# Performance work log

Hardware: AMD Instinct MI355X
Metric: run time of the kernel (lower is better)

The kernel has to match this reference:

```python
import jax, jax.numpy as jnp
import numpy as np

N, E = 40000, 640000
IN, HID, OUT = 128, 128, 128


def _lin(key, fan_in, fan_out):
    bound = 1.0 / np.sqrt(fan_in)
    kw, kb = jax.random.split(key)
    W = jax.random.uniform(kw, (fan_in, fan_out), jnp.float32, -bound, bound)
    b = jax.random.uniform(kb, (fan_out,), jnp.float32, -bound, bound)
    return W, b


def setup_inputs() -> dict:
    key = jax.random.key(0)
    ks = jax.random.split(key, 10)
    node_feat = jax.random.normal(ks[0], (N, IN), jnp.float32)
    coord_feat = jax.random.normal(ks[1], (N, 3), jnp.float32)
    src = jax.random.randint(ks[2], (E,), 0, N, jnp.int32)
    dst = jax.random.randint(ks[3], (E,), 0, N, jnp.int32)
    # edge_mlp: Linear(2*IN+1 -> HID), SiLU, Linear(HID -> HID), SiLU
    We1, be1 = _lin(ks[4], 2 * IN + 1, HID)
    We2, be2 = _lin(ks[5], HID, HID)
    # node_mlp: Linear(IN+HID -> HID), SiLU, Linear(HID -> OUT)
    Wn1, bn1 = _lin(ks[6], IN + HID, HID)
    Wn2, bn2 = _lin(ks[7], HID, OUT)
    # coord_mlp: Linear(HID -> HID), SiLU, Linear(HID -> 1, bias=False)
    Wc1, bc1 = _lin(ks[8], HID, HID)
    Wc2, _ = _lin(ks[9], HID, 1)
    return {"node_feat": node_feat, "coord_feat": coord_feat, "src": src, "dst": dst,
            "We1": We1, "be1": be1, "We2": We2, "be2": be2,
            "Wn1": Wn1, "bn1": bn1, "Wn2": Wn2, "bn2": bn2,
            "Wc1": Wc1, "bc1": bc1, "Wc2": Wc2}


def reference(node_feat, coord_feat, src, dst,
              We1, be1, We2, be2, Wn1, bn1, Wn2, bn2, Wc1, bc1, Wc2):
    n = node_feat.shape[0]
    # edge gather: u_sub_v gives x_src - x_dst
    x_diff = coord_feat[src] - coord_feat[dst]                       # (E, 3)
    dist = jnp.sqrt(jnp.sum(x_diff * x_diff, axis=-1, keepdims=True))  # (E, 1)
    x_dir = x_diff / (dist + 1e-7)
    f = jnp.concatenate([node_feat[src], node_feat[dst], dist], axis=-1)  # (E, 2*IN+1)
    msg_h = jax.nn.silu(jax.nn.silu(f @ We1 + be1) @ We2 + be2)      # (E, HID)
    coef = jax.nn.silu(msg_h @ Wc1 + bc1) @ Wc2                      # (E, 1)
    msg_x = coef * x_dir                                             # (E, 3)
    # scatter-reduce to destination nodes: sum for h, mean for x
    h_neigh = jax.ops.segment_sum(msg_h, dst, num_segments=n)        # (N, HID)
    cnt = jax.ops.segment_sum(jnp.ones((dst.shape[0], 1), msg_x.dtype), dst, num_segments=n)
    x_neigh = jax.ops.segment_sum(msg_x, dst, num_segments=n) / jnp.maximum(cnt, 1.0)
    h = jax.nn.silu(jnp.concatenate([node_feat, h_neigh], axis=-1) @ Wn1 + bn1) @ Wn2 + bn2
    return h, coord_feat + x_neigh
```

## Files before the change

### kernel.cpp

```cpp
#include <hip/hip_runtime.h>
#include <hip/hip_bf16.h>
#include <math.h>
#include <stdint.h>

#define N_NODES 40000
#define N_EDGES 640000

typedef short short8 __attribute__((ext_vector_type(8)));
typedef float f32x4 __attribute__((ext_vector_type(4)));

__device__ __forceinline__ float silu(float x) {
    return __fdividef(x, 1.0f + __expf(-x));
}

__device__ __forceinline__ unsigned short f2bf(float f) {
    unsigned u = __float_as_uint(f);
    u += 0x7FFF + ((u >> 16) & 1);
    return (unsigned short)(u >> 16);
}
__device__ __forceinline__ float bf2f(unsigned short h) {
    return __uint_as_float(((unsigned)h) << 16);
}
__device__ __forceinline__ unsigned pk2bf(float a, float b) {
    __hip_bfloat162 h = __float22bfloat162_rn(make_float2(a, b));
    unsigned u;
    __builtin_memcpy(&u, &h, 4);
    return u;
}

__global__ __launch_bounds__(1024) void k_scanA(const int* __restrict__ deg,
                                                int* __restrict__ rsl,
                                                int* __restrict__ btot) {
    __shared__ int wsum[16];
    const int t = threadIdx.x;
    const int lane = t & 63, wid = t >> 6;
    const int base = blockIdx.x * 1000;
    const int x0 = (t < 1000) ? deg[base + t] : 0;
    int x = x0;
#pragma unroll
    for (int s = 1; s < 64; s <<= 1) {
        const int u = __shfl_up(x, s, 64);
        if (lane >= s) x += u;
    }
    if (lane == 63) wsum[wid] = x;
    __syncthreads();
    if (wid == 0) {
        int ws = (lane < 16) ? wsum[lane] : 0;
#pragma unroll
        for (int s = 1; s < 16; s <<= 1) {
            const int u = __shfl_up(ws, s, 64);
            if (lane >= s) ws += u;
        }
        if (lane < 16) wsum[lane] = ws;
    }
    __syncthreads();
    const int wbase = (wid > 0) ? wsum[wid - 1] : 0;
    if (t < 1000) rsl[base + t] = wbase + x - x0;
    if (t == 0) btot[blockIdx.x] = wsum[15];
}

__global__ __launch_bounds__(256) void k_fill(const int* __restrict__ dst,
                                              const int* __restrict__ rsl,
                                              const int* __restrict__ btot,
                                              int* __restrict__ cursor,
                                              int* __restrict__ elist) {
    __shared__ int sbo[40];
    const int t = threadIdx.x;
    if (t < 64) {
        const int x0 = (t < 40) ? btot[t] : 0;
        int x = x0;
#pragma unroll
        for (int s = 1; s < 64; s <<= 1) {
            const int u = __shfl_up(x, s, 64);
            if (t >= s) x += u;
        }
        if (t < 40) sbo[t] = x - x0;
    }
    __syncthreads();
    const int e = blockIdx.x * 256 + t;
    if (e < N_EDGES) {
        const int d = dst[e];
        const int p = atomicAdd(&cursor[d], 1);
        elist[sbo[d / 1000] + rsl[d] + p] = e;
    }
}

__global__ __launch_bounds__(128) void k_pack2(
    const float* __restrict__ We1, const float* __restrict__ We2,
    const float* __restrict__ Wc1, const float* __restrict__ Wn1,
    const float* __restrict__ Wn2,
    unsigned short* __restrict__ Wt_e1, unsigned short* __restrict__ Wt_e2,
    unsigned short* __restrict__ Wt_c1, unsigned short* __restrict__ Wt_n1,
    unsigned short* __restrict__ Wt_n2,
    int* __restrict__ deg, int* __restrict__ cursor, float* __restrict__ xs,
    float* __restrict__ hn) {
    const int b = blockIdx.x;
    const int t = threadIdx.x;
    Wt_e1[b * 128 + t] = f2bf(We1[(size_t)((b >> 7) * 128 + t) * 128 + (b & 127)]);
    if (b < 128) {
        Wt_e2[b * 128 + t] = f2bf(We2[(size_t)t * 128 + b]);
        Wt_c1[b * 128 + t] = f2bf(Wc1[(size_t)t * 128 + b]);
        Wt_n2[b * 128 + t] = f2bf(Wn2[(size_t)t * 128 + b]);
        Wt_n1[b * 256 + t] = f2bf(Wn1[(size_t)t * 128 + b]);
        Wt_n1[b * 256 + 128 + t] = f2bf(Wn1[(size_t)(128 + t) * 128 + b]);
    }
    const int gid = b * 128 + t;
    for (int i = gid; i < N_NODES; i += 32768) { deg[i] = 0; cursor[i] = 0; }
    for (int i = gid; i < N_NODES * 4; i += 32768) xs[i] = 0.0f;
    float4* hz = (float4*)hn;
    const float4 z4 = {0.f, 0.f, 0.f, 0.f};
    for (int i = gid; i < N_NODES * 32; i += 32768) hz[i] = z4;
}

__global__ __launch_bounds__(256) void k_cntpre(
    const float* __restrict__ nf, const unsigned short* __restrict__ Wt_e1,
    const float* __restrict__ be1,
    unsigned short* __restrict__ Pc,
    const int* __restrict__ dst, int* __restrict__ deg) {
    __shared__ __align__(16) unsigned short sNF[32][136];
    const int t = threadIdx.x;
    const int node0 = blockIdx.x * 32;
    {
        const int e0 = (blockIdx.x * 256 + t) * 2;
        const int d0 = dst[e0], d1 = dst[e0 + 1];
        atomicAdd(&deg[d0], 1);
        atomicAdd(&deg[d1], 1);
    }
    {
        const int m = t >> 3, kc = (t & 7) * 16;
        const float* sp = &nf[(size_t)(node0 + m) * 128 + kc];
        const float4 v0 = *(const float4*)(sp + 0);
        const float4 v1 = *(const float4*)(sp + 4);
        const float4 v2 = *(const float4*)(sp + 8);
        const float4 v3 = *(const float4*)(sp + 12);
        int4 o0, o1;
        o0.x = pk2bf(v0.x, v0.y); o0.y = pk2bf(v0.z, v0.w);
        o0.z = pk2bf(v1.x, v1.y); o0.w = pk2bf(v1.z, v1.w);
        o1.x = pk2bf(v2.x, v2.y); o1.y = pk2bf(v2.z, v2.w);
        o1.z = pk2bf(v3.x, v3.y); o1.w = pk2bf(v3.z, v3.w);
        *(int4*)&sNF[m][kc] = o0;
        *(int4*)&sNF[m][kc + 8] = o1;
    }
    __syncthreads();

    const int w = t >> 6, l = t & 63, c = l & 15, quad = l >> 4;
    const int n0 = w * 64;

    f32x4 acc[2][4];
#pragma unroll
    for (int mt = 0; mt < 2; mt++)
#pragma unroll
        for (int tl = 0; tl < 4; tl++) acc[mt][tl] = (f32x4){0.f, 0.f, 0.f, 0.f};

#pragma unroll
    for (int k0 = 0; k0 < 128; k0 += 32) {
        const short8 a0 = *(const short8*)&sNF[c][k0 + quad * 8];
        const short8 a1 = *(const short8*)&sNF[16 + c][k0 + quad * 8];
#pragma unroll
        for (int tl = 0; tl < 4; tl++) {
            const short8 b = *(const short8*)(Wt_e1 +
                ((size_t)(n0 + tl * 16 + c) << 7) + k0 + quad * 8);
            acc[0][tl] = __builtin_amdgcn_mfma_f32_16x16x32_bf16(a0, b, acc[0][tl], 0, 0, 0);
            acc[1][tl] = __builtin_amdgcn_mfma_f32_16x16x32_bf16(a1, b, acc[1][tl], 0, 0, 0);
        }
    }
#pragma unroll
    for (int mt = 0; mt < 2; mt++)
#pragma unroll
        for (int tl = 0; tl < 4; tl++) {
            const int col = n0 + tl * 16 + c;
            const float bias = (col >= 128) ? be1[col - 128] : 0.0f;
            const unsigned p01 = pk2bf(acc[mt][tl][0] + bias, acc[mt][tl][1] + bias);
            const unsigned p23 = pk2bf(acc[mt][tl][2] + bias, acc[mt][tl][3] + bias);
            const int row = node0 + mt * 16 + quad * 4;
            Pc[(size_t)(row + 0) * 256 + col] = (unsigned short)p01;
            Pc[(size_t)(row + 1) * 256 + col] = (unsigned short)(p01 >> 16);
            Pc[(size_t)(row + 2) * 256 + col] = (unsigned short)p23;
            Pc[(size_t)(row + 3) * 256 + col] = (unsigned short)(p23 >> 16);
        }
}

__global__ __launch_bounds__(256) void k_edge9(
    const unsigned short* __restrict__ Pc, const float* __restrict__ coord,
    const int* __restrict__ src, const int* __restrict__ dst,
    const int* __restrict__ elist,
    const float* __restrict__ We1,
    const unsigned short* __restrict__ Wt_e2, const float* __restrict__ be2,
    const unsigned short* __restrict__ Wt_c1, const float* __restrict__ bc1,
    const float* __restrict__ Wc2,
    float* __restrict__ h_neigh, float* __restrict__ xs) {
    __shared__ __align__(16) unsigned short sT[64][136];
    __shared__ float scoefp[4][32];
    __shared__ float sw[128];
    __shared__ float sdist[64];
    __shared__ float sxd[64][3];
    __shared__ int ssrc[64];
    __shared__ int sdst[64];

    const int t = threadIdx.x;
    const int bid = (int)blockIdx.x;
    const int swz = (bid & 7) * 1250 + (bid >> 3);
    const int e0 = swz * 64;

    if (t < 64) {
        const int eid = elist[e0 + t];
        const int s = src[eid], d = dst[eid];
        ssrc[t] = s; sdst[t] = d;
        const float dx = coord[3 * s + 0] - coord[3 * d + 0];
        const float dy = coord[3 * s + 1] - coord[3 * d + 1];
        const float dz = coord[3 * s + 2] - coord[3 * d + 2];
        const float dist = sqrtf(dx * dx + dy * dy + dz * dz);
        sdist[t] = dist;
        const float inv = __fdividef(1.0f, dist + 1e-7f);
        sxd[t][0] = dx * inv; sxd[t][1] = dy * inv; sxd[t][2] = dz * inv;
    } else if (t < 96) {
        ((float4*)sw)[t - 64] = ((const float4*)(We1 + 256 * 128))[t - 64];
    }
    __syncthreads();

    {
        const int e = t >> 2;
        const int kc = (t & 3) * 32;
        const int s = ssrc[e], d = sdst[e];
        const float dist = sdist[e];
        const unsigned short* p1 = Pc + (size_t)s * 256 + kc;
        const unsigned short* p2 = Pc + (size_t)d * 256 + 128 + kc;
        short8 a[4], b[4];
#pragma unroll
        for (int i = 0; i < 4; i++) {
            a[i] = *(const short8*)(p1 + i * 8);
            b[i] = *(const short8*)(p2 + i * 8);
        }
#pragma unroll
        for (int i = 0; i < 4; i++) {
            float v[8];
#pragma unroll
            for (int kk = 0; kk < 8; kk++) {
                const int k = kc + i * 8 + kk;
                v[kk] = silu(bf2f((unsigned short)a[i][kk]) + bf2f((unsigned short)b[i][kk])
                             + dist * sw[k]);
            }
            int4 o;
            o.x = pk2bf(v[0], v[1]); o.y = pk2bf(v[2], v[3]);
            o.z = pk2bf(v[4], v[5]); o.w = pk2bf(v[6], v[7]);
            *(int4*)&sT[e][kc + i * 8] = o;
        }
    }
    __syncthreads();

    const int w = t >> 6;
    const int l = t & 63;
    const int h = w & 1;
    const int H = w >> 1;
    const int m0 = h * 32;
    const int n0 = H * 64;
    const int c = l & 15;
    const int quad = l >> 4;

    f32x4 acc1[2][4];
#pragma unroll
    for (int mt = 0; mt < 2; mt++)
#pragma unroll
        for (int tile = 0; tile < 4; tile++) acc1[mt][tile] = (f32x4){0.f, 0.f, 0.f, 0.f};
#pragma unroll
    for (int k0 = 0; k0 < 128; k0 += 32) {
        const short8 a0 = *(const short8*)&sT[m0 + c][k0 + quad * 8];
        const short8 a1 = *(const short8*)&sT[m0 + 16 + c][k0 + quad * 8];
#pragma unroll
        for (int tile = 0; tile < 4; tile++) {
            const short8 b = *(const short8*)(Wt_e2 +
                ((size_t)(n0 + tile * 16 + c) << 7) + k0 + quad * 8);
            acc1[0][tile] = __builtin_amdgcn_mfma_f32_16x16x32_bf16(a0, b, acc1[0][tile], 0, 0, 0);
            acc1[1][tile] = __builtin_amdgcn_mfma_f32_16x16x32_bf16(a1, b, acc1[1][tile], 0, 0, 0);
        }
    }
    __syncthreads();

#pragma unroll
    for (int mt = 0; mt < 2; mt++)
#pragma unroll
        for (int tile = 0; tile < 4; tile++) {
            const int col = n0 + tile * 16 + c;
            const float bb = be2[col];
            const unsigned p01 = pk2bf(silu(acc1[mt][tile][0] + bb), silu(acc1[mt][tile][1] + bb));
            const unsigned p23 = pk2bf(silu(acc1[mt][tile][2] + bb), silu(acc1[mt][tile][3] + bb));
            const int row = m0 + mt * 16 + quad * 4;
            sT[row + 0][col] = (unsigned short)p01;
            sT[row + 1][col] = (unsigned short)(p01 >> 16);
            sT[row + 2][col] = (unsigned short)p23;
            sT[row + 3][col] = (unsigned short)(p23 >> 16);
        }
    __syncthreads();

    {
        const int j = t & 127;
        const int q = t >> 7;
        const int eb = q * 32;
        float aA = bf2f(sT[eb][j]);      int pA = sdst[eb];
        float aB = bf2f(sT[eb + 16][j]); int pB = sdst[eb + 16];
#pragma unroll
        for (int i = 1; i < 16; i++) {
            const int dA = sdst[eb + i];
            const int dB = sdst[eb + 16 + i];
            const float vA = bf2f(sT[eb + i][j]);
            const float vB = bf2f(sT[eb + 16 + i][j]);
            if (dA != pA) { atomicAdd(&h_neigh[(size_t)pA * 128 + j], aA); aA = 0.f; pA = dA; }
            aA += vA;
            if (dB != pB) { atomicAdd(&h_neigh[(size_t)pB * 128 + j], aB); aB = 0.f; pB = dB; }
            aB += vB;
        }
        atomicAdd(&h_neigh[(size_t)pA * 128 + j], aA);
        atomicAdd(&h_neigh[(size_t)pB * 128 + j], aB);
    }

    {
        f32x4 acc[2][4];
#pragma unroll
        for (int mt = 0; mt < 2; mt++)
#pragma unroll
            for (int tile = 0; tile < 4; tile++) acc[mt][tile] = (f32x4){0.f, 0.f, 0.f, 0.f};
#pragma unroll
        for (int k0 = 0; k0 < 128; k0 += 32) {
            const short8 a0 = *(const short8*)&sT[m0 + c][k0 + quad * 8];
            const short8 a1 = *(const short8*)&sT[m0 + 16 + c][k0 + quad * 8];
#pragma unroll
            for (int tile = 0; tile < 4; tile++) {
                const short8 b = *(const short8*)(Wt_c1 +
                    ((size_t)(n0 + tile * 16 + c) << 7) + k0 + quad * 8);
                acc[0][tile] = __builtin_amdgcn_mfma_f32_16x16x32_bf16(a0, b, acc[0][tile], 0, 0, 0);
                acc[1][tile] = __builtin_amdgcn_mfma_f32_16x16x32_bf16(a1, b, acc[1][tile], 0, 0, 0);
            }
        }
        float part[2][4] = {{0.f, 0.f, 0.f, 0.f}, {0.f, 0.f, 0.f, 0.f}};
#pragma unroll
        for (int tile = 0; tile < 4; tile++) {
            const int col = n0 + tile * 16 + c;
            const float bc = bc1[col];
            const float wc = Wc2[col];
#pragma unroll
            for (int mt = 0; mt < 2; mt++)
#pragma unroll
                for (int r = 0; r < 4; r++)
                    part[mt][r] += silu(acc[mt][tile][r] + bc) * wc;
        }
#pragma unroll
        for (int off = 1; off < 16; off <<= 1) {
#pragma unroll
            for (int mt = 0; mt < 2; mt++)
#pragma unroll
                for (int r = 0; r < 4; r++)
                    part[mt][r] += __shfl_xor(part[mt][r], off, 64);
        }
        if (c == 0) {
#pragma unroll
            for (int mt = 0; mt < 2; mt++)
#pragma unroll
                for (int r = 0; r < 4; r++)
                    scoefp[w][mt * 16 + quad * 4 + r] = part[mt][r];
        }
    }

    if (l < 32) {
        const int e = h * 32 + l;
        const int d = sdst[e];
        const float cf = scoefp[w][l];
        float v0 = cf * sxd[e][0];
        float v1 = cf * sxd[e][1];
        float v2 = cf * sxd[e][2];
#pragma unroll
        for (int s = 1; s < 32; s <<= 1) {
            const float u0 = __shfl_down(v0, s, 64);
            const float u1 = __shfl_down(v1, s, 64);
            const float u2 = __shfl_down(v2, s, 64);
            const int ud = __shfl_down(d, s, 64);
            if (l + s < 32 && ud == d) { v0 += u0; v1 += u1; v2 += u2; }
        }
        if (l == 0 || sdst[e - 1] != d) {
            atomicAdd(&xs[(size_t)d * 4 + 0], v0);
            atomicAdd(&xs[(size_t)d * 4 + 1], v1);
            atomicAdd(&xs[(size_t)d * 4 + 2], v2);
        }
    }
}

__global__ __launch_bounds__(256) void k_node(
    const float* __restrict__ nf, const float* __restrict__ coord,
    const float* __restrict__ hn, const float* __restrict__ xs,
    const int* __restrict__ deg,
    const unsigned short* __restrict__ Wt_n1, const float* __restrict__ bn1,
    const unsigned short* __restrict__ Wt_n2, const float* __restrict__ bn2,
    float* __restrict__ out_h, float* __restrict__ out_x) {
    __shared__ __align__(16) unsigned short sAB[32][264];
    __shared__ __align__(16) unsigned short sH[32][136];
    const int t = threadIdx.x;
    const int node0 = blockIdx.x * 32;
    {
        const int m = t >> 3, kc = (t & 7) * 32;
        const float* base = (kc < 128) ? &nf[(size_t)(node0 + m) * 128 + kc]
                                       : &hn[(size_t)(node0 + m) * 128 + (kc - 128)];
#pragma unroll
        for (int kk = 0; kk < 32; kk += 8) {
            const float4 v0 = *(const float4*)(base + kk);
            const float4 v1 = *(const float4*)(base + kk + 4);
            int4 o;
            o.x = pk2bf(v0.x, v0.y); o.y = pk2bf(v0.z, v0.w);
            o.z = pk2bf(v1.x, v1.y); o.w = pk2bf(v1.z, v1.w);
            *(int4*)&sAB[m][kc + kk] = o;
        }
    }
    if (t < 96) {
        const int m = t / 3, cc = t - m * 3;
        const int i = node0 + m;
        const float cnt = (float)deg[i];
        out_x[(size_t)i * 3 + cc] =
            coord[(size_t)i * 3 + cc] + __fdividef(xs[(size_t)i * 4 + cc], fmaxf(cnt, 1.0f));
    }
    __syncthreads();

    const int w = t >> 6, l = t & 63, c = l & 15, quad = l >> 4;
    const int n0 = w * 32;

    {
        f32x4 acc[2][2];
#pragma unroll
        for (int mt = 0; mt < 2; mt++)
#pragma unroll
            for (int tl = 0; tl < 2; tl++) acc[mt][tl] = (f32x4){0.f, 0.f, 0.f, 0.f};
#pragma unroll
        for (int k0 = 0; k0 < 256; k0 += 32) {
            const short8 a0 = *(const short8*)&sAB[c][k0 + quad * 8];
            const short8 a1 = *(const short8*)&sAB[16 + c][k0 + quad * 8];
#pragma unroll
            for (int tl = 0; tl < 2; tl++) {
                const short8 b = *(const short8*)(Wt_n1 +
                    ((size_t)(n0 + tl * 16 + c) << 8) + k0 + quad * 8);
                acc[0][tl] = __builtin_amdgcn_mfma_f32_16x16x32_bf16(a0, b, acc[0][tl], 0, 0, 0);
                acc[1][tl] = __builtin_amdgcn_mfma_f32_16x16x32_bf16(a1, b, acc[1][tl], 0, 0, 0);
            }
        }
#pragma unroll
        for (int mt = 0; mt < 2; mt++)
#pragma unroll
            for (int tl = 0; tl < 2; tl++) {
                const int col = n0 + tl * 16 + c;
                const float bb = bn1[col];
                const unsigned p01 = pk2bf(silu(acc[mt][tl][0] + bb), silu(acc[mt][tl][1] + bb));
                const unsigned p23 = pk2bf(silu(acc[mt][tl][2] + bb), silu(acc[mt][tl][3] + bb));
                const int row = mt * 16 + quad * 4;
                sH[row + 0][col] = (unsigned short)p01;
                sH[row + 1][col] = (unsigned short)(p01 >> 16);
                sH[row + 2][col] = (unsigned short)p23;
                sH[row + 3][col] = (unsigned short)(p23 >> 16);
            }
    }
    __syncthreads();

    {
        f32x4 acc[2][2];
#pragma unroll
        for (int mt = 0; mt < 2; mt++)
#pragma unroll
            for (int tl = 0; tl < 2; tl++) acc[mt][tl] = (f32x4){0.f, 0.f, 0.f, 0.f};
#pragma unroll
        for (int k0 = 0; k0 < 128; k0 += 32) {
            const short8 a0 = *(const short8*)&sH[c][k0 + quad * 8];
            const short8 a1 = *(const short8*)&sH[16 + c][k0 + quad * 8];
#pragma unroll
            for (int tl = 0; tl < 2; tl++) {
                const short8 b = *(const short8*)(Wt_n2 +
                    ((size_t)(n0 + tl * 16 + c) << 7) + k0 + quad * 8);
                acc[0][tl] = __builtin_amdgcn_mfma_f32_16x16x32_bf16(a0, b, acc[0][tl], 0, 0, 0);
                acc[1][tl] = __builtin_amdgcn_mfma_f32_16x16x32_bf16(a1, b, acc[1][tl], 0, 0, 0);
            }
        }
#pragma unroll
        for (int mt = 0; mt < 2; mt++)
#pragma unroll
            for (int tl = 0; tl < 2; tl++) {
                const int col = n0 + tl * 16 + c;
                const float bb = bn2[col];
#pragma unroll
                for (int r = 0; r < 4; r++) {
                    const int row = mt * 16 + quad * 4 + r;
                    out_h[(size_t)(node0 + row) * 128 + col] = acc[mt][tl][r] + bb;
                }
            }
    }
}

extern "C" void kernel_launch(void* const* d_in, const int* in_sizes, int n_in,
                              void* d_out, int out_size, void* d_ws, size_t ws_size,
                              hipStream_t stream) {
    const float* nf    = (const float*)d_in[0];
    const float* coord = (const float*)d_in[1];
    const int*   src   = (const int*)d_in[2];
    const int*   dst   = (const int*)d_in[3];
    const float* We1   = (const float*)d_in[4];
    const float* be1   = (const float*)d_in[5];
    const float* We2   = (const float*)d_in[6];
    const float* be2   = (const float*)d_in[7];
    const float* Wn1   = (const float*)d_in[8];
    const float* bn1   = (const float*)d_in[9];
    const float* Wn2   = (const float*)d_in[10];
    const float* bn2   = (const float*)d_in[11];
    const float* Wc1   = (const float*)d_in[12];
    const float* bc1   = (const float*)d_in[13];
    const float* Wc2   = (const float*)d_in[14];

    unsigned short* Pc = (unsigned short*)d_ws;
    float* hn = (float*)(Pc + (size_t)N_NODES * 256);
    float* xs = hn + (size_t)N_NODES * 128;
    int* deg       = (int*)(xs + (size_t)N_NODES * 4);
    int* rsl       = deg + N_NODES;
    int* cursor    = rsl + N_NODES;
    int* btot      = cursor + N_NODES;
    int* elist     = btot + 64;
    unsigned short* Wt_e1 = (unsigned short*)
        (((uintptr_t)(elist + N_EDGES) + 255) & ~(uintptr_t)255);
    unsigned short* Wt_e2 = Wt_e1 + 256 * 128;
    unsigned short* Wt_c1 = Wt_e2 + 128 * 128;
    unsigned short* Wt_n1 = Wt_c1 + 128 * 128;
    unsigned short* Wt_n2 = Wt_n1 + 128 * 256;

    float* out_h = (float*)d_out;
    float* out_x = out_h + (size_t)N_NODES * 128;

    k_pack2<<<256, 128, 0, stream>>>(We1, We2, Wc1, Wn1, Wn2,
                                     Wt_e1, Wt_e2, Wt_c1, Wt_n1, Wt_n2,
                                     deg, cursor, xs, hn);
    k_cntpre<<<N_NODES / 32, 256, 0, stream>>>(nf, Wt_e1, be1, Pc, dst, deg);
    k_scanA<<<40, 1024, 0, stream>>>(deg, rsl, btot);
    k_fill<<<(N_EDGES + 255) / 256, 256, 0, stream>>>(dst, rsl, btot, cursor, elist);
    k_edge9<<<N_EDGES / 64, 256, 0, stream>>>(Pc, coord, src, dst, elist,
                                              We1, Wt_e2, be2, Wt_c1, bc1,
                                              Wc2, hn, xs);
    k_node<<<N_NODES / 32, 256, 0, stream>>>(nf, coord, hn, xs, deg,
                                             Wt_n1, bn1, Wt_n2, bn2, out_h, out_x);
}
```

Baseline: 413.4 us.

## Make each wavefront own 16 edges and keep first MLP activations in registers

The edge kernel is reorganized so each of the four wavefronts handles its own 16 edges across all 128 output columns, instead of splitting a 64-edge tile in 2x2 across waves. The first-layer SiLU activations are built straight into MFMA A-operand registers rather than staged through shared memory, and the distance weight row is read from global memory. This removes several block-wide barriers and shared-memory round trips, relying on wave-local lgkmcnt waits. In exchange each wave loads the full Wt_e2 and Wt_c1 B operands (twice the weight traffic per edge), and the correctness of the wave-local waits depends on each wave only touching its own shared rows.

```diff
diff --git a/kernel.cpp b/kernel.cpp
--- a/kernel.cpp
+++ b/kernel.cpp
@@ -180,7 +180,7 @@
         }
 }
 
-__global__ __launch_bounds__(256) void k_edge9(
+__global__ __launch_bounds__(256) void k_edge10(
     const unsigned short* __restrict__ Pc, const float* __restrict__ coord,
     const int* __restrict__ src, const int* __restrict__ dst,
     const int* __restrict__ elist,
@@ -190,120 +190,103 @@
     const float* __restrict__ Wc2,
     float* __restrict__ h_neigh, float* __restrict__ xs) {
     __shared__ __align__(16) unsigned short sT[64][136];
-    __shared__ float scoefp[4][32];
-    __shared__ float sw[128];
+    __shared__ float scoef[4][16];
     __shared__ float sdist[64];
     __shared__ float sxd[64][3];
     __shared__ int ssrc[64];
     __shared__ int sdst[64];
 
     const int t = threadIdx.x;
+    const int w = t >> 6, l = t & 63;
+    const int c = l & 15, quad = l >> 4;
     const int bid = (int)blockIdx.x;
     const int swz = (bid & 7) * 1250 + (bid >> 3);
     const int e0 = swz * 64;
-
-    if (t < 64) {
-        const int eid = elist[e0 + t];
+    const int eb = w * 16;
+
+    if (l < 16) {
+        const int eid = elist[e0 + eb + l];
         const int s = src[eid], d = dst[eid];
-        ssrc[t] = s; sdst[t] = d;
+        ssrc[eb + l] = s; sdst[eb + l] = d;
         const float dx = coord[3 * s + 0] - coord[3 * d + 0];
         const float dy = coord[3 * s + 1] - coord[3 * d + 1];
         const float dz = coord[3 * s + 2] - coord[3 * d + 2];
         const float dist = sqrtf(dx * dx + dy * dy + dz * dz);
-        sdist[t] = dist;
+        sdist[eb + l] = dist;
         const float inv = __fdividef(1.0f, dist + 1e-7f);
-        sxd[t][0] = dx * inv; sxd[t][1] = dy * inv; sxd[t][2] = dz * inv;
-    } else if (t < 96) {
-        ((float4*)sw)[t - 64] = ((const float4*)(We1 + 256 * 128))[t - 64];
-    }
-    __syncthreads();
-
-    {
-        const int e = t >> 2;
-        const int kc = (t & 3) * 32;
-        const int s = ssrc[e], d = sdst[e];
-        const float dist = sdist[e];
-        const unsigned short* p1 = Pc + (size_t)s * 256 + kc;
-        const unsigned short* p2 = Pc + (size_t)d * 256 + 128 + kc;
-        short8 a[4], b[4];
-#pragma unroll
-        for (int i = 0; i < 4; i++) {
-            a[i] = *(const short8*)(p1 + i * 8);
-            b[i] = *(const short8*)(p2 + i * 8);
-        }
-#pragma unroll
-        for (int i = 0; i < 4; i++) {
+        sxd[eb + l][0] = dx * inv; sxd[eb + l][1] = dy * inv; sxd[eb + l][2] = dz * inv;
+    }
+    asm volatile("s_waitcnt lgkmcnt(0)" ::: "memory");
+
+    short8 aQ[4];
+    {
+        const int er = eb + c;
+        const int s = ssrc[er], d = sdst[er];
+        const float dist = sdist[er];
+        const unsigned short* p1 = Pc + (size_t)s * 256 + quad * 8;
+        const unsigned short* p2 = Pc + (size_t)d * 256 + 128 + quad * 8;
+        const float* wd = We1 + 256 * 128 + quad * 8;
+#pragma unroll
+        for (int k0 = 0; k0 < 4; k0++) {
+            const short8 a = *(const short8*)(p1 + k0 * 32);
+            const short8 b = *(const short8*)(p2 + k0 * 32);
+            const float4 w0 = *(const float4*)(wd + k0 * 32);
+            const float4 w1 = *(const float4*)(wd + k0 * 32 + 4);
             float v[8];
-#pragma unroll
-            for (int kk = 0; kk < 8; kk++) {
-                const int k = kc + i * 8 + kk;
-                v[kk] = silu(bf2f((unsigned short)a[i][kk]) + bf2f((unsigned short)b[i][kk])
-                             + dist * sw[k]);
-            }
+            v[0] = silu(bf2f((unsigned short)a[0]) + bf2f((unsigned short)b[0]) + dist * w0.x);
+            v[1] = silu(bf2f((unsigned short)a[1]) + bf2f((unsigned short)b[1]) + dist * w0.y);
+            v[2] = silu(bf2f((unsigned short)a[2]) + bf2f((unsigned short)b[2]) + dist * w0.z);
+            v[3] = silu(bf2f((unsigned short)a[3]) + bf2f((unsigned short)b[3]) + dist * w0.w);
+            v[4] = silu(bf2f((unsigned short)a[4]) + bf2f((unsigned short)b[4]) + dist * w1.x);
+            v[5] = silu(bf2f((unsigned short)a[5]) + bf2f((unsigned short)b[5]) + dist * w1.y);
+            v[6] = silu(bf2f((unsigned short)a[6]) + bf2f((unsigned short)b[6]) + dist * w1.z);
+            v[7] = silu(bf2f((unsigned short)a[7]) + bf2f((unsigned short)b[7]) + dist * w1.w);
             int4 o;
             o.x = pk2bf(v[0], v[1]); o.y = pk2bf(v[2], v[3]);
             o.z = pk2bf(v[4], v[5]); o.w = pk2bf(v[6], v[7]);
-            *(int4*)&sT[e][kc + i * 8] = o;
-        }
-    }
-    __syncthreads();
-
-    const int w = t >> 6;
-    const int l = t & 63;
-    const int h = w & 1;
-    const int H = w >> 1;
-    const int m0 = h * 32;
-    const int n0 = H * 64;
-    const int c = l & 15;
-    const int quad = l >> 4;
-
-    f32x4 acc1[2][4];
-#pragma unroll
-    for (int mt = 0; mt < 2; mt++)
-#pragma unroll
-        for (int tile = 0; tile < 4; tile++) acc1[mt][tile] = (f32x4){0.f, 0.f, 0.f, 0.f};
-#pragma unroll
-    for (int k0 = 0; k0 < 128; k0 += 32) {
-        const short8 a0 = *(const short8*)&sT[m0 + c][k0 + quad * 8];
-        const short8 a1 = *(const short8*)&sT[m0 + 16 + c][k0 + quad * 8];
-#pragma unroll
-        for (int tile = 0; tile < 4; tile++) {
+            __builtin_memcpy(&aQ[k0], &o, 16);
+        }
+    }
+
+    f32x4 acc1[8];
+#pragma unroll
+    for (int tl = 0; tl < 8; tl++) acc1[tl] = (f32x4){0.f, 0.f, 0.f, 0.f};
+#pragma unroll
+    for (int k0 = 0; k0 < 4; k0++) {
+#pragma unroll
+        for (int tl = 0; tl < 8; tl++) {
             const short8 b = *(const short8*)(Wt_e2 +
-                ((size_t)(n0 + tile * 16 + c) << 7) + k0 + quad * 8);
-            acc1[0][tile] = __builtin_amdgcn_mfma_f32_16x16x32_bf16(a0, b, acc1[0][tile], 0, 0, 0);
-            acc1[1][tile] = __builtin_amdgcn_mfma_f32_16x16x32_bf16(a1, b, acc1[1][tile], 0, 0, 0);
-        }
-    }
-    __syncthreads();
-
-#pragma unroll
-    for (int mt = 0; mt < 2; mt++)
-#pragma unroll
-        for (int tile = 0; tile < 4; tile++) {
-            const int col = n0 + tile * 16 + c;
-            const float bb = be2[col];
-            const unsigned p01 = pk2bf(silu(acc1[mt][tile][0] + bb), silu(acc1[mt][tile][1] + bb));
-            const unsigned p23 = pk2bf(silu(acc1[mt][tile][2] + bb), silu(acc1[mt][tile][3] + bb));
-            const int row = m0 + mt * 16 + quad * 4;
-            sT[row + 0][col] = (unsigned short)p01;
-            sT[row + 1][col] = (unsigned short)(p01 >> 16);
-            sT[row + 2][col] = (unsigned short)p23;
-            sT[row + 3][col] = (unsigned short)(p23 >> 16);
-        }
+                ((size_t)(tl * 16 + c) << 7) + k0 * 32 + quad * 8);
+            acc1[tl] = __builtin_amdgcn_mfma_f32_16x16x32_bf16(aQ[k0], b, acc1[tl], 0, 0, 0);
+        }
+    }
+
+#pragma unroll
+    for (int tl = 0; tl < 8; tl++) {
+        const int col = tl * 16 + c;
+        const float bb = be2[col];
+        const unsigned p01 = pk2bf(silu(acc1[tl][0] + bb), silu(acc1[tl][1] + bb));
+        const unsigned p23 = pk2bf(silu(acc1[tl][2] + bb), silu(acc1[tl][3] + bb));
+        const int row = eb + quad * 4;
+        sT[row + 0][col] = (unsigned short)p01;
+        sT[row + 1][col] = (unsigned short)(p01 >> 16);
+        sT[row + 2][col] = (unsigned short)p23;
+        sT[row + 3][col] = (unsigned short)(p23 >> 16);
+    }
     __syncthreads();
 
     {
         const int j = t & 127;
         const int q = t >> 7;
-        const int eb = q * 32;
-        float aA = bf2f(sT[eb][j]);      int pA = sdst[eb];
-        float aB = bf2f(sT[eb + 16][j]); int pB = sdst[eb + 16];
+        const int ebq = q * 32;
+        float aA = bf2f(sT[ebq][j]);      int pA = sdst[ebq];
+        float aB = bf2f(sT[ebq + 16][j]); int pB = sdst[ebq + 16];
 #pragma unroll
         for (int i = 1; i < 16; i++) {
-            const int dA = sdst[eb + i];
-            const int dB = sdst[eb + 16 + i];
-            const float vA = bf2f(sT[eb + i][j]);
-            const float vB = bf2f(sT[eb + 16 + i][j]);
+            const int dA = sdst[ebq + i];
+            const int dB = sdst[ebq + 16 + i];
+            const float vA = bf2f(sT[ebq + i][j]);
+            const float vB = bf2f(sT[ebq + 16 + i][j]);
             if (dA != pA) { atomicAdd(&h_neigh[(size_t)pA * 128 + j], aA); aA = 0.f; pA = dA; }
             aA += vA;
             if (dB != pB) { atomicAdd(&h_neigh[(size_t)pB * 128 + j], aB); aB = 0.f; pB = dB; }
@@ -314,71 +297,66 @@
     }
 
     {
-        f32x4 acc[2][4];
-#pragma unroll
-        for (int mt = 0; mt < 2; mt++)
-#pragma unroll
-            for (int tile = 0; tile < 4; tile++) acc[mt][tile] = (f32x4){0.f, 0.f, 0.f, 0.f};
-#pragma unroll
-        for (int k0 = 0; k0 < 128; k0 += 32) {
-            const short8 a0 = *(const short8*)&sT[m0 + c][k0 + quad * 8];
-            const short8 a1 = *(const short8*)&sT[m0 + 16 + c][k0 + quad * 8];
-#pragma unroll
-            for (int tile = 0; tile < 4; tile++) {
+        short8 a2[4];
+#pragma unroll
+        for (int k0 = 0; k0 < 4; k0++)
+            a2[k0] = *(const short8*)&sT[eb + c][k0 * 32 + quad * 8];
+
+        f32x4 acc2[8];
+#pragma unroll
+        for (int tl = 0; tl < 8; tl++) acc2[tl] = (f32x4){0.f, 0.f, 0.f, 0.f};
+#pragma unroll
+        for (int k0 = 0; k0 < 4; k0++) {
+#pragma unroll
+            for (int tl = 0; tl < 8; tl++) {
                 const short8 b = *(const short8*)(Wt_c1 +
-                    ((size_t)(n0 + tile * 16 + c) << 7) + k0 + quad * 8);
-                acc[0][tile] = __builtin_amdgcn_mfma_f32_16x16x32_bf16(a0, b, acc[0][tile], 0, 0, 0);
-                acc[1][tile] = __builtin_amdgcn_mfma_f32_16x16x32_bf16(a1, b, acc[1][tile], 0, 0, 0);
+                    ((size_t)(tl * 16 + c) << 7) + k0 * 32 + quad * 8);
+                acc2[tl] = __builtin_amdgcn_mfma_f32_16x16x32_bf16(a2[k0], b, acc2[tl], 0, 0, 0);
             }
         }
-        float part[2][4] = {{0.f, 0.f, 0.f, 0.f}, {0.f, 0.f, 0.f, 0.f}};
-#pragma unroll
-        for (int tile = 0; tile < 4; tile++) {
-            const int col = n0 + tile * 16 + c;
+        float part[4] = {0.f, 0.f, 0.f, 0.f};
+#pragma unroll
+        for (int tl = 0; tl < 8; tl++) {
+            const int col = tl * 16 + c;
             const float bc = bc1[col];
             const float wc = Wc2[col];
 #pragma unroll
-            for (int mt = 0; mt < 2; mt++)
-#pragma unroll
-                for (int r = 0; r < 4; r++)
-                    part[mt][r] += silu(acc[mt][tile][r] + bc) * wc;
+            for (int r = 0; r < 4; r++)
+                part[r] += silu(acc2[tl][r] + bc) * wc;
         }
 #pragma unroll
         for (int off = 1; off < 16; off <<= 1) {
 #pragma unroll
-            for (int mt = 0; mt < 2; mt++)
-#pragma unroll
-                for (int r = 0; r < 4; r++)
-                    part[mt][r] += __shfl_xor(part[mt][r], off, 64);
+            for (int r = 0; r < 4; r++)
+                part[r] += __shfl_xor(part[r], off, 64);
         }
         if (c == 0) {
 #pragma unroll
-            for (int mt = 0; mt < 2; mt++)
-#pragma unroll
-                for (int r = 0; r < 4; r++)
-                    scoefp[w][mt * 16 + quad * 4 + r] = part[mt][r];
-        }
-    }
-
-    if (l < 32) {
-        const int e = h * 32 + l;
-        const int d = sdst[e];
-        const float cf = scoefp[w][l];
+            for (int r = 0; r < 4; r++)
+                scoef[w][quad * 4 + r] = part[r];
+        }
+    }
+    asm volatile("s_waitcnt lgkmcnt(0)" ::: "memory");
+
+    if (l < 16) {
+        const int e = eb + l;
+        const int dd = sdst[e];
+        const float cf = scoef[w][l];
         float v0 = cf * sxd[e][0];
         float v1 = cf * sxd[e][1];
         float v2 = cf * sxd[e][2];
 #pragma unroll
-        for (int s = 1; s < 32; s <<= 1) {
+        for (int s = 1; s < 16; s <<= 1) {
             const float u0 = __shfl_down(v0, s, 64);
             const float u1 = __shfl_down(v1, s, 64);
             const float u2 = __shfl_down(v2, s, 64);
-            const int ud = __shfl_down(d, s, 64);
-            if (l + s < 32 && ud == d) { v0 += u0; v1 += u1; v2 += u2; }
-        }
-        if (l == 0 || sdst[e - 1] != d) {
-            atomicAdd(&xs[(size_t)d * 4 + 0], v0);
-            atomicAdd(&xs[(size_t)d * 4 + 1], v1);
-            atomicAdd(&xs[(size_t)d * 4 + 2], v2);
+            const int ud = __shfl_down(dd, s, 64);
+            if (l + s < 16 && ud == dd) { v0 += u0; v1 += u1; v2 += u2; }
+        }
+        if (e == 0 || sdst[e - 1] != dd) {
+            atomicAdd(&xs[(size_t)dd * 4 + 0], v0);
+            atomicAdd(&xs[(size_t)dd * 4 + 1], v1);
+            atomicAdd(&xs[(size_t)dd * 4 + 2], v2);
         }
     }
 }
@@ -531,9 +509,9 @@
     k_cntpre<<<N_NODES / 32, 256, 0, stream>>>(nf, Wt_e1, be1, Pc, dst, deg);
     k_scanA<<<40, 1024, 0, stream>>>(deg, rsl, btot);
     k_fill<<<(N_EDGES + 255) / 256, 256, 0, stream>>>(dst, rsl, btot, cursor, elist);
-    k_edge9<<<N_EDGES / 64, 256, 0, stream>>>(Pc, coord, src, dst, elist,
-                                              We1, Wt_e2, be2, Wt_c1, bc1,
-                                              Wc2, hn, xs);
+    k_edge10<<<N_EDGES / 64, 256, 0, stream>>>(Pc, coord, src, dst, elist,
+                                               We1, Wt_e2, be2, Wt_c1, bc1,
+                                               Wc2, hn, xs);
     k_node<<<N_NODES / 32, 256, 0, stream>>>(nf, coord, hn, xs, deg,
                                              Wt_n1, bn1, Wt_n2, bn2, out_h, out_x);
 }
```

After: 553.3 us. +33.9%, slower.
